# Performance work log

Hardware: AMD Instinct MI355X
Metric: run time of the kernel (lower is better)

## Reference

```python
import jax, jax.numpy as jnp
import numpy as np

GROUPS = 32
EPS = 1e-5


def group_norm(x, gamma, beta):
    b, h, w, c = x.shape
    xg = x.reshape(b, h, w, GROUPS, c // GROUPS)
    mean = jnp.mean(xg, axis=(1, 2, 4), keepdims=True)
    var = jnp.var(xg, axis=(1, 2, 4), keepdims=True)
    xn = ((xg - mean) * jax.lax.rsqrt(var + EPS)).reshape(b, h, w, c)
    return xn * gamma + beta


def conv1x1(x, w, b):
    # 1x1 conv == per-pixel dense: [b,h,w,c] x [c,d] -> [b,h,w,d]
    return jnp.einsum('bhwc,cd->bhwd', x, w) + b


def setup_inputs() -> dict:
    key = jax.random.key(0)
    ks = jax.random.split(key, 6)
    B, H, W, C = 4, 64, 64, 512
    s = 1.0 / np.sqrt(C)
    return {
        'x': jax.random.normal(ks[0], (B, H, W, C), jnp.float32),
        'gn_gamma': jnp.ones((C,), jnp.float32),
        'gn_beta': jnp.zeros((C,), jnp.float32),
        'wq': jax.random.normal(ks[1], (C, C), jnp.float32) * s,
        'bq': jnp.zeros((C,), jnp.float32),
        'wk': jax.random.normal(ks[2], (C, C), jnp.float32) * s,
        'bk': jnp.zeros((C,), jnp.float32),
        'wv': jax.random.normal(ks[3], (C, C), jnp.float32) * s,
        'bv': jnp.zeros((C,), jnp.float32),
        'wp': jax.random.normal(ks[4], (C, C), jnp.float32) * s,
        'bp': jnp.zeros((C,), jnp.float32),
    }


def reference(x, gn_gamma, gn_beta, wq, bq, wk, bk, wv, bv, wp, bp):
    b, h, w, c = x.shape
    n = h * w
    h_ = group_norm(x, gn_gamma, gn_beta)
    q = conv1x1(h_, wq, bq).reshape(b, n, c)
    k = conv1x1(h_, wk, bk).reshape(b, n, c)
    v = conv1x1(h_, wv, bv).reshape(b, n, c)
    scale = c ** (-0.5)
    scores = jnp.einsum('bic,bjc->bij', q, k) * scale  # [b, n, n]
    attn = jax.nn.softmax(scores, axis=-1)
    out = jnp.einsum('bij,bjc->bic', attn, v).reshape(b, h, w, c)
    return x + conv1x1(out, wp, bp)
```

## Files before the change

kernel.cpp:

```cpp
#include <hip/hip_runtime.h>
#include <cstdint>


typedef __bf16 bf16_t;
typedef bf16_t bf16x8 __attribute__((ext_vector_type(8)));
typedef float floatx4 __attribute__((ext_vector_type(4)));
typedef int v8i __attribute__((ext_vector_type(8)));

__device__ __forceinline__ uint16_t f2b(float f) {
    uint32_t u = __builtin_bit_cast(uint32_t, f);
    u += 0x7fffu + ((u >> 16) & 1u);
    return (uint16_t)(u >> 16);
}
__device__ __forceinline__ float b2f(uint16_t h) {
    uint32_t u = ((uint32_t)h) << 16;
    return __builtin_bit_cast(float, u);
}
__device__ __forceinline__ unsigned pk_fp8x4(float a, float b, float c, float d) {
    int w = __builtin_amdgcn_cvt_pk_fp8_f32(a, b, 0, false);
    w = __builtin_amdgcn_cvt_pk_fp8_f32(c, d, w, true);
    return (unsigned)w;
}

__device__ __forceinline__ void lds_copy16(void* lds, const void* glob) {
    __builtin_amdgcn_global_load_lds(
        (__attribute__((address_space(1))) void*)(void*)glob,
        (__attribute__((address_space(3))) void*)lds,
        16, 0, 0);
}

__global__ __launch_bounds__(256) void gn_stats(const float* __restrict__ x,
                                                float* __restrict__ stats) {
    const int bg = blockIdx.x;
    const int tid = threadIdx.x;
    const int b = bg >> 5, g = bg & 31;
    const float* base = x + (long)b * (4096L * 512) + g * 16;
    float s = 0.f, sq = 0.f;
    #pragma unroll 8
    for (int i = 0; i < 64; i++) {
        int idx4 = tid + i * 256;
        int pixel = idx4 >> 2, c4 = idx4 & 3;
        const float4 v = *(const float4*)(base + (long)pixel * 512 + c4 * 4);
        s += v.x + v.y + v.z + v.w;
        sq += v.x * v.x + v.y * v.y + v.z * v.z + v.w * v.w;
    }
    #pragma unroll
    for (int off = 32; off > 0; off >>= 1) {
        s += __shfl_down(s, off);
        sq += __shfl_down(sq, off);
    }
    __shared__ float rs[4], rq[4];
    const int lane = tid & 63, w = tid >> 6;
    if (lane == 0) { rs[w] = s; rq[w] = sq; }
    __syncthreads();
    if (tid == 0) {
        float S = rs[0] + rs[1] + rs[2] + rs[3];
        float Q = rq[0] + rq[1] + rq[2] + rq[3];
        float mean = S * (1.f / 65536.f);
        float var = Q * (1.f / 65536.f) - mean * mean;
        stats[bg * 2 + 0] = mean;
        stats[bg * 2 + 1] = rsqrtf(var + 1e-5f);
    }
}

__global__ __launch_bounds__(256) void gn_apply(const float* __restrict__ x,
                                                const float* __restrict__ stats,
                                                const float* __restrict__ gamma,
                                                const float* __restrict__ beta,
                                                uint16_t* __restrict__ h) {
    const long idx4 = (long)blockIdx.x * 256 + threadIdx.x;
    const long e0 = idx4 * 4;
    const int c = (int)(e0 & 511);
    const int b = (int)(e0 >> 21);
    const float2 st = ((const float2*)stats)[b * 32 + (c >> 4)];
    const float4 v = ((const float4*)x)[idx4];
    const float4 gm = ((const float4*)gamma)[c >> 2];
    const float4 bt = ((const float4*)beta)[c >> 2];
    union { ushort4 u; uint16_t s[4]; } o;
    o.s[0] = f2b((v.x - st.x) * st.y * gm.x + bt.x);
    o.s[1] = f2b((v.y - st.x) * st.y * gm.y + bt.y);
    o.s[2] = f2b((v.z - st.x) * st.y * gm.z + bt.z);
    o.s[3] = f2b((v.w - st.x) * st.y * gm.w + bt.w);
    ((ushort4*)h)[idx4] = o.u;
}

__global__ __launch_bounds__(256) void wcast_transpose(const float* __restrict__ w0,
                                                       const float* __restrict__ w1,
                                                       const float* __restrict__ w2,
                                                       const float* __restrict__ w3,
                                                       uint16_t* __restrict__ out) {
    const float* ws[4] = {w0, w1, w2, w3};
    const float* w = ws[blockIdx.z];
    uint16_t* o = out + (long)blockIdx.z * 512 * 512;
    __shared__ uint16_t t[64][65];
    const int nb = blockIdx.x * 64, kb = blockIdx.y * 64;
    const int lc = threadIdx.x & 63, lg = threadIdx.x >> 6;
    #pragma unroll
    for (int i = 0; i < 16; i++) {
        int r = lg * 16 + i;
        t[lc][r] = f2b(w[(long)(kb + r) * 512 + nb + lc]);
    }
    __syncthreads();
    #pragma unroll
    for (int i = 0; i < 16; i++) {
        int r = lg * 16 + i;
        o[(long)(nb + r) * 512 + kb + lc] = t[r][lc];
    }
}

__global__ __launch_bounds__(256) void qkv_gemm(const uint16_t* __restrict__ h,
                                                const uint16_t* __restrict__ wT,
                                                const float* __restrict__ bq,
                                                const float* __restrict__ bk,
                                                const float* __restrict__ bv,
                                                uint8_t* __restrict__ q,
                                                uint8_t* __restrict__ k,
                                                uint8_t* __restrict__ vt) {
    __shared__ __align__(16) uint16_t smem[128 * 136];
    uint16_t* sA = smem;
    uint16_t* sB = smem + 8192;

    const int tid = threadIdx.x;
    const long m0 = (long)blockIdx.y * 128;
    const int n0 = blockIdx.x * 128;

    const int lane = tid & 63;
    const int wave = tid >> 6;
    const int wm = (wave & 1) * 64;
    const int wn = (wave >> 1) * 64;
    const int fr = lane & 15;
    const int fh = lane >> 4;
    const int sw = fr & 7;

    floatx4 acc[4][4];
    #pragma unroll
    for (int i = 0; i < 4; i++)
        #pragma unroll
        for (int j = 0; j < 4; j++) acc[i][j] = (floatx4){0.f, 0.f, 0.f, 0.f};

    for (int kt = 0; kt < 512; kt += 64) {
        __syncthreads();
        #pragma unroll
        for (int i = 0; i < 4; i++) {
            const int c = i * 256 + tid;
            const int row = c >> 3;
            const int gj = (c & 7) ^ (row & 7);
            lds_copy16(&sA[c * 8], h + (m0 + row) * 512L + kt + gj * 8);
            lds_copy16(&sB[c * 8], wT + (n0 + row) * 512L + kt + gj * 8);
        }
        __syncthreads();
        #pragma unroll
        for (int kk = 0; kk < 64; kk += 32) {
            const int jx = ((fh + (kk >> 3)) ^ sw) * 8;
            bf16x8 av[4], bv_[4];
            #pragma unroll
            for (int mi = 0; mi < 4; mi++)
                av[mi] = *(const bf16x8*)&sA[(wm + mi * 16 + fr) * 64 + jx];
            #pragma unroll
            for (int ni = 0; ni < 4; ni++)
                bv_[ni] = *(const bf16x8*)&sB[(wn + ni * 16 + fr) * 64 + jx];
            #pragma unroll
            for (int mi = 0; mi < 4; mi++)
                #pragma unroll
                for (int ni = 0; ni < 4; ni++)
                    acc[mi][ni] = __builtin_amdgcn_mfma_f32_16x16x32_bf16(
                        av[mi], bv_[ni], acc[mi][ni], 0, 0, 0);
        }
    }

    const int quad = lane >> 4;
    const int w = n0 >> 9;
    const int nc = n0 & 511;
    const float* bias = (w == 0) ? bq : (w == 1) ? bk : bv;
    __syncthreads();
    if (w < 2) {
        #pragma unroll
        for (int ni = 0; ni < 4; ni++) {
            const int col_l = wn + ni * 16 + fr;
            const float bb = bias[nc + col_l];
            #pragma unroll
            for (int mi = 0; mi < 4; mi++) {
                #pragma unroll
                for (int r = 0; r < 4; r++) {
                    const int row_l = wm + mi * 16 + quad * 4 + r;
                    smem[row_l * 136 + col_l] = f2b(acc[mi][ni][r] + bb);
                }
            }
        }
        __syncthreads();
        uint8_t* out = (w == 0) ? q : k;
        #pragma unroll
        for (int it = 0; it < 8; it++) {
            const int row_l = it * 16 + (tid >> 4);
            const int c0 = (tid & 15) * 8;
            const uint4 d = *(const uint4*)&smem[row_l * 136 + c0];
            const uint16_t* e = (const uint16_t*)&d;
            uint2 o;
            o.x = pk_fp8x4(b2f(e[0]), b2f(e[1]), b2f(e[2]), b2f(e[3]));
            o.y = pk_fp8x4(b2f(e[4]), b2f(e[5]), b2f(e[6]), b2f(e[7]));
            *(uint2*)&out[(m0 + row_l) * 512 + nc + c0] = o;
        }
    } else {
        uint8_t* s8 = (uint8_t*)smem;
        #pragma unroll
        for (int ni = 0; ni < 4; ni++) {
            const int ch_l = wn + ni * 16 + fr;
            const float bb = bias[nc + ch_l];
            #pragma unroll
            for (int mi = 0; mi < 4; mi++) {
                const int pix0 = wm + mi * 16 + quad * 4;
                *(unsigned*)&s8[ch_l * 144 + pix0] =
                    pk_fp8x4(acc[mi][ni][0] + bb, acc[mi][ni][1] + bb,
                             acc[mi][ni][2] + bb, acc[mi][ni][3] + bb);
            }
        }
        __syncthreads();
        const long b = m0 >> 12;
        const int pixb = (int)(m0 & 4095);
        uint8_t* vtb = vt + b * (512L * 4096);
        #pragma unroll
        for (int it = 0; it < 4; it++) {
            const int ch_l = it * 32 + (tid >> 3);
            const int p0 = (tid & 7) * 16;
            *(uint4*)&vtb[(long)(nc + ch_l) * 4096 + pixb + p0] =
                *(const uint4*)&s8[ch_l * 144 + p0];
        }
    }
}

__global__ __launch_bounds__(512, 2) void flash_attn(const uint8_t* __restrict__ q8,
                                                     const uint8_t* __restrict__ k8,
                                                     const uint8_t* __restrict__ vt8,
                                                     uint16_t* __restrict__ ao) {
    __shared__ __align__(16) uint8_t sK[2][65536];
    __shared__ __align__(16) uint8_t Pl[8192];
    __shared__ float lpart[8][32];
    __shared__ float linv[64];
    uint16_t* obuf = (uint16_t*)sK;

    const int tid = threadIdx.x;
    const int lane = tid & 63;
    const int wave = tid >> 6;
    const int fr = lane & 15;
    const int quad = lane >> 4;
    const int sw = fr & 7;

    const int lb = ((blockIdx.x & 7) << 5) | (blockIdx.x >> 3);
    const int batch = lb >> 6;
    const int mt = lb & 63;
    const long qbase = (long)batch * 4096 + mt * 64;

    const int wr = wave >> 2;
    const int wcg = wave & 3;
    const int wm = wr * 32;
    const int wc = wcg * 32;
    const float qscale = 0.06375871540654937f;

    v8i aQ[2][4];
    #pragma unroll
    for (int mi = 0; mi < 2; mi++) {
        const uint8_t* qp = q8 + (qbase + wm + mi * 16 + fr) * 512 + quad * 32;
        #pragma unroll
        for (int kt = 0; kt < 4; kt++) {
            const uint4 lo = *(const uint4*)(qp + kt * 128);
            const uint4 hi = *(const uint4*)(qp + kt * 128 + 16);
            aQ[mi][kt] = (v8i){(int)lo.x, (int)lo.y, (int)lo.z, (int)lo.w,
                               (int)hi.x, (int)hi.y, (int)hi.z, (int)hi.w};
        }
    }
    const uint8_t* kbb = k8 + (long)batch * (4096L * 512);
    const uint8_t* vrow = vt8 + (long)batch * (512L * 4096) +
                          (long)(wave * 64 + fr) * 4096 + quad * 32;

    floatx4 oacc[4][4];
    #pragma unroll
    for (int i = 0; i < 4; i++)
        #pragma unroll
        for (int j = 0; j < 4; j++) oacc[i][j] = (floatx4){0.f, 0.f, 0.f, 0.f};
    float lsum[2][4];
    #pragma unroll
    for (int i = 0; i < 2; i++)
        #pragma unroll
        for (int r = 0; r < 4; r++) lsum[i][r] = 0.f;

#define STAGE(t_, buf_)                                                        \
    do {                                                                       \
        const uint8_t* kb = kbb + (long)(t_) * (128L * 512);                   \
        uint8_t* dst = &sK[buf_][0];                                           \
        _Pragma("unroll")                                                      \
        for (int i = 0; i < 8; i++) {                                          \
            const int chunk = i * 512 + tid;                                   \
            const int kt = chunk >> 10;                                        \
            const int c = chunk & 1023;                                        \
            const int row = c >> 3;                                            \
            const int gj = (c & 7) ^ (row & 7);                                \
            lds_copy16(dst + kt * 16384 + c * 16,                              \
                       kb + row * 512 + kt * 128 + gj * 16);                   \
        }                                                                      \
    } while (0)

    STAGE(0, 0);

    for (int t = 0; t < 32; t++) {
        const int cur = t & 1;
        __syncthreads();
        v8i bV[4];
        #pragma unroll
        for (int ni = 0; ni < 4; ni++) {
            const uint8_t* vp = vrow + (long)ni * (16L * 4096) + t * 128;
            const uint4 lo = *(const uint4*)vp;
            const uint4 hi = *(const uint4*)(vp + 16);
            bV[ni] = (v8i){(int)lo.x, (int)lo.y, (int)lo.z, (int)lo.w,
                           (int)hi.x, (int)hi.y, (int)hi.z, (int)hi.w};
        }
        if (t < 31) STAGE(t + 1, cur ^ 1);
        floatx4 sacc[2][2];
        #pragma unroll
        for (int mi = 0; mi < 2; mi++)
            #pragma unroll
            for (int ni = 0; ni < 2; ni++) sacc[mi][ni] = (floatx4){0.f, 0.f, 0.f, 0.f};
        #pragma unroll
        for (int kt = 0; kt < 4; kt++) {
            v8i bK[2];
            #pragma unroll
            for (int ni = 0; ni < 2; ni++) {
                const int row = wc + ni * 16 + fr;
                const uint8_t* base = &sK[cur][kt * 16384 + row * 128];
                const uint4 lo = *(const uint4*)(base + (((2 * quad) ^ sw) << 4));
                const uint4 hi = *(const uint4*)(base + (((2 * quad + 1) ^ sw) << 4));
                bK[ni] = (v8i){(int)lo.x, (int)lo.y, (int)lo.z, (int)lo.w,
                               (int)hi.x, (int)hi.y, (int)hi.z, (int)hi.w};
            }
            #pragma unroll
            for (int mi = 0; mi < 2; mi++)
                #pragma unroll
                for (int ni = 0; ni < 2; ni++)
                    sacc[mi][ni] = __builtin_amdgcn_mfma_scale_f32_16x16x128_f8f6f4(
                        aQ[mi][kt], bK[ni], sacc[mi][ni], 0, 0, 0, 0x7f7f7f7fu, 0,
                        0x7f7f7f7fu);
        }
        #pragma unroll
        for (int mi = 0; mi < 2; mi++) {
            #pragma unroll
            for (int ni = 0; ni < 2; ni++) {
                const float p0 = exp2f(sacc[mi][ni][0] * qscale);
                const float p1 = exp2f(sacc[mi][ni][1] * qscale);
                const float p2 = exp2f(sacc[mi][ni][2] * qscale);
                const float p3 = exp2f(sacc[mi][ni][3] * qscale);
                lsum[mi][0] += p0;
                lsum[mi][1] += p1;
                lsum[mi][2] += p2;
                lsum[mi][3] += p3;
                const unsigned pw = pk_fp8x4(p0, p1, p2, p3);
                const int chunk = wcg * 2 + ni;
                #pragma unroll
                for (int r = 0; r < 4; r++) {
                    const int prow = wm + mi * 16 + quad * 4 + r;
                    Pl[prow * 128 + ((chunk ^ (prow & 7)) << 4) + fr] =
                        (uint8_t)(pw >> (8 * r));
                }
            }
        }
        __syncthreads();
        #pragma unroll
        for (int mi = 0; mi < 4; mi++) {
            const int prow = mi * 16 + fr;
            const uint4 lo = *(const uint4*)&Pl[prow * 128 + (((2 * quad) ^ sw) << 4)];
            const uint4 hi = *(const uint4*)&Pl[prow * 128 + (((2 * quad + 1) ^ sw) << 4)];
            const v8i aP = (v8i){(int)lo.x, (int)lo.y, (int)lo.z, (int)lo.w,
                                 (int)hi.x, (int)hi.y, (int)hi.z, (int)hi.w};
            #pragma unroll
            for (int ni = 0; ni < 4; ni++)
                oacc[mi][ni] = __builtin_amdgcn_mfma_scale_f32_16x16x128_f8f6f4(
                    aP, bV[ni], oacc[mi][ni], 0, 0, 0, 0x7f7f7f7fu, 0,
                    0x7f7f7f7fu);
        }
    }
#undef STAGE

    #pragma unroll
    for (int mi = 0; mi < 2; mi++)
        #pragma unroll
        for (int r = 0; r < 4; r++) {
            #pragma unroll
            for (int off = 1; off < 16; off <<= 1)
                lsum[mi][r] += __shfl_xor(lsum[mi][r], off);
        }
    if ((lane & 15) == 0) {
        #pragma unroll
        for (int mi = 0; mi < 2; mi++)
            #pragma unroll
            for (int r = 0; r < 4; r++)
                lpart[wave][mi * 16 + quad * 4 + r] = lsum[mi][r];
    }
    __syncthreads();
    if (tid < 64) {
        const int wr_ = tid >> 5, rl = tid & 31;
        const float L = lpart[wr_ * 4 + 0][rl] + lpart[wr_ * 4 + 1][rl] +
                        lpart[wr_ * 4 + 2][rl] + lpart[wr_ * 4 + 3][rl];
        linv[tid] = __builtin_amdgcn_rcpf(L);
    }
    __syncthreads();
    #pragma unroll
    for (int hh = 0; hh < 2; hh++) {
        if ((wave >> 2) == hh) {
            #pragma unroll
            for (int mi = 0; mi < 4; mi++)
                #pragma unroll
                for (int ni = 0; ni < 4; ni++)
                    #pragma unroll
                    for (int r = 0; r < 4; r++) {
                        const int row = mi * 16 + quad * 4 + r;
                        const int col = (wave & 3) * 64 + ni * 16 + fr;
                        obuf[row * 256 + col] = f2b(oacc[mi][ni][r] * linv[row]);
                    }
        }
        __syncthreads();
        {
            const int srow = tid >> 3;
            const int sc = tid & 7;
            uint16_t* dst = ao + (qbase + srow) * 512 + hh * 256;
            const uint16_t* src = &obuf[srow * 256];
            #pragma unroll
            for (int it = 0; it < 4; it++)
                *(uint4*)(dst + (sc + it * 8) * 8) =
                    *(const uint4*)(src + (sc + it * 8) * 8);
        }
        __syncthreads();
    }
}

__global__ __launch_bounds__(256) void gemm_proj(const uint16_t* __restrict__ A,
                                                 const uint16_t* __restrict__ B,
                                                 float* __restrict__ Cout,
                                                 const float* __restrict__ bias,
                                                 const float* __restrict__ resid) {
    __shared__ __align__(16) uint16_t smem[128 * 136];
    uint16_t* sA = smem;
    uint16_t* sB = smem + 8192;
    const int N = 512;

    const int tid = threadIdx.x;
    const long m0 = (long)blockIdx.y * 128;
    const long n0 = (long)blockIdx.x * 128;

    const int lane = tid & 63;
    const int wave = tid >> 6;
    const int wm = (wave & 1) * 64;
    const int wn = (wave >> 1) * 64;
    const int fr = lane & 15;
    const int fh = lane >> 4;
    const int sw = fr & 7;

    floatx4 acc[4][4];
    #pragma unroll
    for (int i = 0; i < 4; i++)
        #pragma unroll
        for (int j = 0; j < 4; j++) acc[i][j] = (floatx4){0.f, 0.f, 0.f, 0.f};

    for (int kt = 0; kt < 512; kt += 64) {
        __syncthreads();
        #pragma unroll
        for (int i = 0; i < 4; i++) {
            const int c = i * 256 + tid;
            const int row = c >> 3;
            const int gj = (c & 7) ^ (row & 7);
            lds_copy16(&sA[c * 8], A + (m0 + row) * 512L + kt + gj * 8);
            lds_copy16(&sB[c * 8], B + (n0 + row) * 512L + kt + gj * 8);
        }
        __syncthreads();
        #pragma unroll
        for (int kk = 0; kk < 64; kk += 32) {
            const int jx = ((fh + (kk >> 3)) ^ sw) * 8;
            bf16x8 av[4], bv[4];
            #pragma unroll
            for (int mi = 0; mi < 4; mi++)
                av[mi] = *(const bf16x8*)&sA[(wm + mi * 16 + fr) * 64 + jx];
            #pragma unroll
            for (int ni = 0; ni < 4; ni++)
                bv[ni] = *(const bf16x8*)&sB[(wn + ni * 16 + fr) * 64 + jx];
            #pragma unroll
            for (int mi = 0; mi < 4; mi++)
                #pragma unroll
                for (int ni = 0; ni < 4; ni++)
                    acc[mi][ni] = __builtin_amdgcn_mfma_f32_16x16x32_bf16(
                        av[mi], bv[ni], acc[mi][ni], 0, 0, 0);
        }
    }

    const int quad = lane >> 4;
    #pragma unroll
    for (int ni = 0; ni < 4; ni++) {
        const long col = n0 + wn + ni * 16 + fr;
        const float bv_ = bias[col];
        #pragma unroll
        for (int mi = 0; mi < 4; mi++) {
            #pragma unroll
            for (int r = 0; r < 4; r++) {
                const long row = m0 + wm + mi * 16 + quad * 4 + r;
                Cout[row * N + col] = acc[mi][ni][r] + bv_ + resid[row * N + col];
            }
        }
    }
}

extern "C" void kernel_launch(void* const* d_in, const int* in_sizes, int n_in,
                              void* d_out, int out_size, void* d_ws, size_t ws_size,
                              hipStream_t stream) {
    const float* x  = (const float*)d_in[0];
    const float* gg = (const float*)d_in[1];
    const float* gb = (const float*)d_in[2];
    const float* wq = (const float*)d_in[3];
    const float* bq = (const float*)d_in[4];
    const float* wk = (const float*)d_in[5];
    const float* bk = (const float*)d_in[6];
    const float* wv = (const float*)d_in[7];
    const float* bv = (const float*)d_in[8];
    const float* wp = (const float*)d_in[9];
    const float* bp = (const float*)d_in[10];
    float* out = (float*)d_out;

    char* ws = (char*)d_ws;
    size_t off = 0;
    auto alloc = [&](size_t bytes) {
        char* p = ws + off;
        off += (bytes + 255) & ~(size_t)255;
        return p;
    };
    float*    stats = (float*)alloc(128 * 2 * sizeof(float));
    uint16_t* h     = (uint16_t*)alloc(16384L * 512 * 2);
    uint16_t* wT    = (uint16_t*)alloc(4L * 512 * 512 * 2);
    uint8_t*  q8    = (uint8_t*)alloc(16384L * 512);
    uint8_t*  k8    = (uint8_t*)alloc(16384L * 512);
    uint8_t*  vt8   = (uint8_t*)alloc(16384L * 512);
    uint16_t* ao    = (uint16_t*)alloc(16384L * 512 * 2);
    if (off > ws_size) return;

    gn_stats<<<128, 256, 0, stream>>>(x, stats);
    gn_apply<<<8192, 256, 0, stream>>>(x, stats, gg, gb, h);
    wcast_transpose<<<dim3(8, 8, 4), 256, 0, stream>>>(wq, wk, wv, wp, wT);

    qkv_gemm<<<dim3(12, 128), 256, 0, stream>>>(h, wT, bq, bk, bv, q8, k8, vt8);
    flash_attn<<<dim3(256), dim3(512), 0, stream>>>(q8, k8, vt8, ao);
    gemm_proj<<<dim3(4, 128), 256, 0, stream>>>(ao, wT + 3 * 262144, out, bp, x);
}
```

Before: 321.4 us.

## Split attention KV range across two blocks and combine partial outputs

The flash attention kernel now splits the 32 key tiles into two halves, launching 512 blocks instead of 256. Each block writes unnormalized fp32 partial outputs and row sums, and a new combine kernel adds the halves, normalizes, and converts to bf16. K staging drops to a single LDS buffer, with the next stage issued after the P barrier, so each block uses less LDS and occupancy is raised to 4. MFMA sections are wrapped with s_setprio. The cost is extra fp32 global traffic (about 32 MB written and read) and one more launch. The split needs no max-rescaling because the kernel already uses a fixed exponent without a running max.

```diff
diff --git a/kernel.cpp b/kernel.cpp
--- a/kernel.cpp
+++ b/kernel.cpp
@@ -228,15 +228,14 @@
     }
 }
 
-__global__ __launch_bounds__(512, 2) void flash_attn(const uint8_t* __restrict__ q8,
+__global__ __launch_bounds__(512, 4) void flash_attn(const uint8_t* __restrict__ q8,
                                                      const uint8_t* __restrict__ k8,
                                                      const uint8_t* __restrict__ vt8,
-                                                     uint16_t* __restrict__ ao) {
-    __shared__ __align__(16) uint8_t sK[2][65536];
+                                                     float* __restrict__ op,
+                                                     float* __restrict__ lp) {
+    __shared__ __align__(16) uint8_t sK[65536];
     __shared__ __align__(16) uint8_t Pl[8192];
     __shared__ float lpart[8][32];
-    __shared__ float linv[64];
-    uint16_t* obuf = (uint16_t*)sK;
 
     const int tid = threadIdx.x;
     const int lane = tid & 63;
@@ -245,10 +244,13 @@
     const int quad = lane >> 4;
     const int sw = fr & 7;
 
-    const int lb = ((blockIdx.x & 7) << 5) | (blockIdx.x >> 3);
-    const int batch = lb >> 6;
-    const int mt = lb & 63;
+    const int lb = ((blockIdx.x & 7) << 6) | (blockIdx.x >> 3);
+    const int half = lb & 1;
+    const int qt = lb >> 1;
+    const int batch = qt >> 6;
+    const int mt = qt & 63;
     const long qbase = (long)batch * 4096 + mt * 64;
+    const int t0 = half * 16;
 
     const int wr = wave >> 2;
     const int wcg = wave & 3;
@@ -283,10 +285,9 @@
         #pragma unroll
         for (int r = 0; r < 4; r++) lsum[i][r] = 0.f;
 
-#define STAGE(t_, buf_)                                                        \
+#define STAGE(t_)                                                              \
     do {                                                                       \
         const uint8_t* kb = kbb + (long)(t_) * (128L * 512);                   \
-        uint8_t* dst = &sK[buf_][0];                                           \
         _Pragma("unroll")                                                      \
         for (int i = 0; i < 8; i++) {                                          \
             const int chunk = i * 512 + tid;                                   \
@@ -294,15 +295,15 @@
             const int c = chunk & 1023;                                        \
             const int row = c >> 3;                                            \
             const int gj = (c & 7) ^ (row & 7);                                \
-            lds_copy16(dst + kt * 16384 + c * 16,                              \
+            lds_copy16(&sK[kt * 16384 + c * 16],                               \
                        kb + row * 512 + kt * 128 + gj * 16);                   \
         }                                                                      \
     } while (0)
 
-    STAGE(0, 0);
-
-    for (int t = 0; t < 32; t++) {
-        const int cur = t & 1;
+    STAGE(t0);
+
+    for (int tt = 0; tt < 16; tt++) {
+        const int t = t0 + tt;
         __syncthreads();
         v8i bV[4];
         #pragma unroll
@@ -313,19 +314,19 @@
             bV[ni] = (v8i){(int)lo.x, (int)lo.y, (int)lo.z, (int)lo.w,
                            (int)hi.x, (int)hi.y, (int)hi.z, (int)hi.w};
         }
-        if (t < 31) STAGE(t + 1, cur ^ 1);
         floatx4 sacc[2][2];
         #pragma unroll
         for (int mi = 0; mi < 2; mi++)
             #pragma unroll
             for (int ni = 0; ni < 2; ni++) sacc[mi][ni] = (floatx4){0.f, 0.f, 0.f, 0.f};
+        __builtin_amdgcn_s_setprio(1);
         #pragma unroll
         for (int kt = 0; kt < 4; kt++) {
             v8i bK[2];
             #pragma unroll
             for (int ni = 0; ni < 2; ni++) {
                 const int row = wc + ni * 16 + fr;
-                const uint8_t* base = &sK[cur][kt * 16384 + row * 128];
+                const uint8_t* base = &sK[kt * 16384 + row * 128];
                 const uint4 lo = *(const uint4*)(base + (((2 * quad) ^ sw) << 4));
                 const uint4 hi = *(const uint4*)(base + (((2 * quad + 1) ^ sw) << 4));
                 bK[ni] = (v8i){(int)lo.x, (int)lo.y, (int)lo.z, (int)lo.w,
@@ -339,6 +340,7 @@
                         aQ[mi][kt], bK[ni], sacc[mi][ni], 0, 0, 0, 0x7f7f7f7fu, 0,
                         0x7f7f7f7fu);
         }
+        __builtin_amdgcn_s_setprio(0);
         #pragma unroll
         for (int mi = 0; mi < 2; mi++) {
             #pragma unroll
@@ -362,6 +364,8 @@
             }
         }
         __syncthreads();
+        if (tt < 15) STAGE(t + 1);
+        __builtin_amdgcn_s_setprio(1);
         #pragma unroll
         for (int mi = 0; mi < 4; mi++) {
             const int prow = mi * 16 + fr;
@@ -375,6 +379,7 @@
                     aP, bV[ni], oacc[mi][ni], 0, 0, 0, 0x7f7f7f7fu, 0,
                     0x7f7f7f7fu);
         }
+        __builtin_amdgcn_s_setprio(0);
     }
 #undef STAGE
 
@@ -398,36 +403,38 @@
         const int wr_ = tid >> 5, rl = tid & 31;
         const float L = lpart[wr_ * 4 + 0][rl] + lpart[wr_ * 4 + 1][rl] +
                         lpart[wr_ * 4 + 2][rl] + lpart[wr_ * 4 + 3][rl];
-        linv[tid] = __builtin_amdgcn_rcpf(L);
-    }
-    __syncthreads();
-    #pragma unroll
-    for (int hh = 0; hh < 2; hh++) {
-        if ((wave >> 2) == hh) {
-            #pragma unroll
-            for (int mi = 0; mi < 4; mi++)
+        lp[(long)half * 16384 + qbase + tid] = L;
+    }
+    {
+        float* ob = op + ((long)half * 16384 + qbase) * 512;
+        #pragma unroll
+        for (int mi = 0; mi < 4; mi++)
+            #pragma unroll
+            for (int ni = 0; ni < 4; ni++) {
+                const int col = wave * 64 + ni * 16 + fr;
                 #pragma unroll
-                for (int ni = 0; ni < 4; ni++)
-                    #pragma unroll
-                    for (int r = 0; r < 4; r++) {
-                        const int row = mi * 16 + quad * 4 + r;
-                        const int col = (wave & 3) * 64 + ni * 16 + fr;
-                        obuf[row * 256 + col] = f2b(oacc[mi][ni][r] * linv[row]);
-                    }
-        }
-        __syncthreads();
-        {
-            const int srow = tid >> 3;
-            const int sc = tid & 7;
-            uint16_t* dst = ao + (qbase + srow) * 512 + hh * 256;
-            const uint16_t* src = &obuf[srow * 256];
-            #pragma unroll
-            for (int it = 0; it < 4; it++)
-                *(uint4*)(dst + (sc + it * 8) * 8) =
-                    *(const uint4*)(src + (sc + it * 8) * 8);
-        }
-        __syncthreads();
-    }
+                for (int r = 0; r < 4; r++) {
+                    const int row = mi * 16 + quad * 4 + r;
+                    ob[(long)row * 512 + col] = oacc[mi][ni][r];
+                }
+            }
+    }
+}
+
+__global__ __launch_bounds__(256) void attn_combine(const float* __restrict__ op,
+                                                    const float* __restrict__ lp,
+                                                    uint16_t* __restrict__ ao) {
+    const long i4 = (long)blockIdx.x * 256 + threadIdx.x;
+    const long row = (i4 * 4) >> 9;
+    const float4 a = ((const float4*)op)[i4];
+    const float4 b = ((const float4*)(op + 16384L * 512))[i4];
+    const float linv = __builtin_amdgcn_rcpf(lp[row] + lp[16384 + row]);
+    union { ushort4 u; uint16_t s[4]; } o;
+    o.s[0] = f2b((a.x + b.x) * linv);
+    o.s[1] = f2b((a.y + b.y) * linv);
+    o.s[2] = f2b((a.z + b.z) * linv);
+    o.s[3] = f2b((a.w + b.w) * linv);
+    ((ushort4*)ao)[i4] = o.u;
 }
 
 __global__ __launch_bounds__(256) void gemm_proj(const uint16_t* __restrict__ A,
@@ -533,6 +540,8 @@
     uint8_t*  q8    = (uint8_t*)alloc(16384L * 512);
     uint8_t*  k8    = (uint8_t*)alloc(16384L * 512);
     uint8_t*  vt8   = (uint8_t*)alloc(16384L * 512);
+    float*    op    = (float*)alloc(2L * 16384 * 512 * 4);
+    float*    lp    = (float*)alloc(2L * 16384 * 4);
     uint16_t* ao    = (uint16_t*)alloc(16384L * 512 * 2);
     if (off > ws_size) return;
 
@@ -541,6 +550,7 @@
     wcast_transpose<<<dim3(8, 8, 4), 256, 0, stream>>>(wq, wk, wv, wp, wT);
 
     qkv_gemm<<<dim3(12, 128), 256, 0, stream>>>(h, wT, bq, bk, bv, q8, k8, vt8);
-    flash_attn<<<dim3(256), dim3(512), 0, stream>>>(q8, k8, vt8, ao);
+    flash_attn<<<dim3(512), dim3(512), 0, stream>>>(q8, k8, vt8, op, lp);
+    attn_combine<<<8192, 256, 0, stream>>>(op, lp, ao);
     gemm_proj<<<dim3(4, 128), 256, 0, stream>>>(ao, wT + 3 * 262144, out, bp, x);
 }
```

New measurement: 746.6 us. 2.32x slower.
